# Kernel optimization log

Hardware: AMD Instinct MI355X
Metric: run time of the kernel (lower is better)

Reference implementation:

```python
import jax, jax.numpy as jnp
import numpy as np

NHEAD = 8
TOPKS = [16, 8]  # coarse -> fine (indexed by loop i over reversed pyramids)


def _gather_kv(t, idx):
    # t: [b, M, nh, d], idx: [b, N, K, nh] -> gathered [b, N, K, nh, d]
    b, M, nh, d = t.shape
    bi = jnp.arange(b)[:, None, None, None]
    hi = jnp.arange(nh)[None, None, None, :]
    return t[bi, idx, hi]


def _process_level(query, key, value, topk_pos, topk_prev, topk):
    # query: [b, c, h0, w0]; key/value: [b, c, h1, w1] with h1=h0, w1=w0
    bs, c, h0, w0 = query.shape
    _, _, h1, w1 = key.shape
    nh = NHEAD
    d = c // nh
    N = (h0 // 2) * (w0 // 2)
    # b c h w -> b (h w) nh d
    k = key.reshape(bs, c, h1 * w1).transpose(0, 2, 1).reshape(bs, h1 * w1, nh, d)
    v = value.reshape(bs, c, h1 * w1).transpose(0, 2, 1).reshape(bs, h1 * w1, nh, d)
    # b c (h 2) (w 2) -> b (h w) 4 nh d  (2x2 query groups)
    q = query.reshape(bs, c, h0 // 2, 2, w0 // 2, 2)
    q = q.transpose(0, 2, 4, 3, 5, 1).reshape(bs, N, 4, nh, d)
    # expand each coarse candidate position into its 2x2 children in the key grid
    tp = topk_pos * 2  # [2, b, N, Kp, nh]
    idx = jnp.stack([(tp[0] + x) * w1 + (tp[1] + y)
                     for x in (0, 1) for y in (0, 1)], axis=3)  # [b,N,Kp,4,nh]
    K = topk_prev * 4
    idx = idx.reshape(bs, N, K, nh)
    # sparse scores: QK[b,n,t,k,h] = <q[b,n,t,h,:], key[b, idx[b,n,k,h], h, :]>
    kg = _gather_kv(k, idx)  # [b,N,K,nh,d]
    QK = jnp.einsum('bnthd,bnkhd->bntkh', q, kg) * (d ** -0.5)
    A = jax.nn.softmax(QK, axis=-2)  # softmax over the K candidates
    # top-k over candidates (dim=-2 of A); lax.top_k works on last axis
    A_t = jnp.swapaxes(A, -1, -2)  # [b,N,4,nh,K]
    ts_t, li = jax.lax.top_k(A_t, topk)
    idx_bc = jnp.broadcast_to(jnp.swapaxes(idx, -1, -2)[:, :, None], A_t.shape)
    ti_t = jnp.take_along_axis(idx_bc, li, axis=-1)
    topk_score = jnp.swapaxes(ts_t, -1, -2)  # [b,N,4,topk,nh]
    topk_idx = jnp.swapaxes(ti_t, -1, -2)
    # value aggregation (idx is repeated over the 4 group slots in the original,
    # so a single gather is the same math): message[b,n,t,h,d]=sum_k A*v[idx]
    vg = _gather_kv(v, idx)  # [b,N,K,nh,d]
    message = jnp.einsum('bntkh,bnkhd->bnthd', A, vg)  # [b,N,4,nh,d]

    def regroup(x):  # b (h w) (t1 t2) k nh -> b (h t1 w t2) k nh
        x = x.reshape(bs, h0 // 2, w0 // 2, 2, 2, topk, nh)
        return x.transpose(0, 1, 3, 2, 4, 5, 6).reshape(bs, h0 * w0, topk, nh)

    return message, regroup(topk_score), regroup(topk_idx)


def _forward(q_fine, q_coarse, k_fine, k_coarse, v_fine, v_coarse, weight, topk_pos):
    queries = [q_fine, q_coarse]  # original list order: fine -> coarse
    keys = [k_fine, k_coarse]
    values = [v_fine, v_coarse]
    messages = []
    topk = TOPKS[0]
    tp = topk_pos
    for i, (q, k, v) in enumerate(zip(queries[::-1], keys[::-1], values[::-1])):
        w1 = k.shape[3]
        topk_prev, topk = topk, TOPKS[i]
        msg, ts, ti = _process_level(q, k, v, tp, topk_prev, topk)
        messages.append(msg)
        tp = jnp.stack([ti // w1, ti % w1])  # (row, col) in current key grid
    wsm = jax.nn.softmax(weight)

    def comb(x, H):  # b (H W) (t1 t2) h d -> b (H t1 W t2) h d, t1=t2=2
        bs, N, _, nh, d = x.shape
        W = N // H
        x = x.reshape(bs, H, W, 2, 2, nh, d).transpose(0, 1, 3, 2, 4, 5, 6)
        return x.reshape(bs, H * 2 * W * 2, nh, d)

    fm = None
    for i, m in enumerate(messages):
        if i == 0:
            fm = m * wsm[i]
        else:
            fm = fm[:, :, None] + m * wsm[i]
        # faithful to original: queries[-i] (note queries[-0] == queries[0])
        H = queries[-i].shape[2]
        fm = comb(fm, H)
    return fm  # [b, Hf*Wf, nh, d]


def setup_inputs() -> dict:
    key = jax.random.key(0)
    ks = jax.random.split(key, 8)
    f = jnp.float32
    return {
        'q_fine': jax.random.normal(ks[0], (2, 128, 128, 128), f),
        'q_coarse': jax.random.normal(ks[1], (2, 128, 64, 64), f),
        'k_fine': jax.random.normal(ks[2], (2, 128, 128, 128), f),
        'k_coarse': jax.random.normal(ks[3], (2, 128, 64, 64), f),
        'v_fine': jax.random.normal(ks[4], (2, 128, 128, 128), f),
        'v_coarse': jax.random.normal(ks[5], (2, 128, 64, 64), f),
        'weight': jax.random.normal(ks[6], (2,), f),
        'topk_pos': jax.random.randint(ks[7], (2, 2, 1024, 16, 8), 0, 32, dtype=jnp.int32),
    }


def reference(q_fine, q_coarse, k_fine, k_coarse, v_fine, v_coarse, weight, topk_pos):
    return _forward(q_fine, q_coarse, k_fine, k_coarse, v_fine, v_coarse, weight, topk_pos)
```

## Files before the change

kernel.cpp:

```cpp
#include <hip/hip_runtime.h>

#define C 128

__device__ __forceinline__ void wave_sync() {
  __builtin_amdgcn_wave_barrier();
  asm volatile("s_waitcnt lgkmcnt(0)" ::: "memory");
  __builtin_amdgcn_wave_barrier();
}

__device__ __forceinline__ void transpose_tile32(const float* __restrict__ in,
                                                 float* __restrict__ out, int P,
                                                 int tx, int chQ, int b,
                                                 float (*tile)[65]) {
  int posBase = tx * 64;
  int chBase  = chQ * 32;
  int tid = threadIdx.x;
  int lp = tid & 63;
  int lr = tid >> 6;
  const float* ip = in + (size_t)b * C * P;
  float* op = out + (size_t)b * C * P;
#pragma unroll
  for (int it = 0; it < 8; ++it) {
    int ch = lr + it * 4;
    tile[ch][lp] = ip[(size_t)(chBase + ch) * P + posBase + lp];
  }
  __syncthreads();
  int dd   = tid & 15;
  int hh2  = (tid >> 4) & 1;
  int prow = tid >> 5;
  int h = (chBase >> 4) + hh2;
#pragma unroll
  for (int it = 0; it < 8; ++it) {
    int pos = prow + it * 8;
    op[((size_t)h * P + posBase + pos) * 16 + dd] = tile[hh2 * 16 + dd][pos];
  }
}

__global__ __launch_bounds__(256) void transpose_coarse(
    const float* __restrict__ q, const float* __restrict__ k,
    const float* __restrict__ v, float* __restrict__ qo,
    float* __restrict__ ko, float* __restrict__ vo) {
  __shared__ alignas(16) float tile[32][65];
  int idx = blockIdx.x;
  int tx = idx & 63;
  int ty = (idx >> 6) % 12;
  int tz = idx / 768;
  int sel = ty >> 2;
  const float* in = sel == 0 ? q : sel == 1 ? k : v;
  float* out      = sel == 0 ? qo : sel == 1 ? ko : vo;
  transpose_tile32(in, out, 4096, tx, ty & 3, tz, tile);
}

__global__ __launch_bounds__(256) void fused_mid(
    const float* __restrict__ qf, const float* __restrict__ kf,
    const float* __restrict__ vf, float* __restrict__ qtf,
    float* __restrict__ ktf, float* __restrict__ vtf,
    const float* __restrict__ qt, const float* __restrict__ kt,
    const float* __restrict__ vt, const int* __restrict__ parents,
    float* __restrict__ mc, int* __restrict__ ti_out)
{
  __shared__ alignas(16) float lds[32 * 65];

  if (blockIdx.x >= 4096) {
    int idx = blockIdx.x - 4096;
    int tx = idx & 255;
    int ty = (idx >> 8) % 12;
    int tz = idx / 3072;
    int sel = ty >> 2;
    const float* in = sel == 0 ? qf : sel == 1 ? kf : vf;
    float* out      = sel == 0 ? qtf : sel == 1 ? ktf : vtf;
    transpose_tile32(in, out, 16384, tx, ty & 3, tz, (float (*)[65])lds);
    return;
  }

  float (*als_k)[4][17][4] = (float (*)[4][17][4])lds;
  float (*qls)[4][16]      = (float (*)[4][16])(lds + 1088);
  int   (*cofs)[64]        = (int (*)[64])    (lds + 1344);

  const int abid = blockIdx.x;
  const int lane = threadIdx.x & 63;
  const int wid  = threadIdx.x >> 6;
  const int wg = (abid & 7) * 512 + (abid >> 3);
  const int u  = wg * 4 + wid;
  const int n  = u & 1023;
  const int bh = u >> 10;
  const int b  = bh >> 3;
  const int h  = bh & 7;
  const int hb = n >> 5;
  const int wb = n & 31;
  const int hD = h * 16;

  { int t = lane >> 4, dd = lane & 15;
    int pix = (hb * 2 + (t >> 1)) * 64 + (wb * 2 + (t & 1));
    qls[wid][t][dd] = qt[((size_t)bh * 4096 + pix) * 16 + dd]; }
  int cand, off0;
  { int kp = lane >> 2, c = lane & 3;
    int r  = parents[(size_t)b * 131072          + n * 128 + kp * 8 + h];
    int cc = parents[(size_t)b * 131072 + 262144 + n * 128 + kp * 8 + h];
    cand = (2 * r + (c >> 1)) * 64 + 2 * cc + (c & 1);
    off0 = (bh * 4096 + cand) * 16;
    cofs[wid][lane] = off0; }
  wave_sync();

  const float4* kv4 = (const float4*)(kt + off0);
  float4 k0 = kv4[0], k1 = kv4[1], k2 = kv4[2], k3 = kv4[3];
  float sc[4];
#pragma unroll
  for (int t = 0; t < 4; ++t) {
    const float4* qv = (const float4*)qls[wid][t];
    float4 q0 = qv[0], q1 = qv[1], q2 = qv[2], q3 = qv[3];
    float acc = k0.x*q0.x + k0.y*q0.y + k0.z*q0.z + k0.w*q0.w
              + k1.x*q1.x + k1.y*q1.y + k1.z*q1.z + k1.w*q1.w
              + k2.x*q2.x + k2.y*q2.y + k2.z*q2.z + k2.w*q2.w
              + k3.x*q3.x + k3.y*q3.y + k3.z*q3.z + k3.w*q3.w;
    sc[t] = acc * 0.25f;
  }

  float mx[4], ex[4], sm[4], a[4];
#pragma unroll
  for (int t = 0; t < 4; ++t) mx[t] = sc[t];
#pragma unroll
  for (int off = 32; off >= 1; off >>= 1)
#pragma unroll
    for (int t = 0; t < 4; ++t) mx[t] = fmaxf(mx[t], __shfl_xor(mx[t], off));
#pragma unroll
  for (int t = 0; t < 4; ++t) { ex[t] = __expf(sc[t] - mx[t]); sm[t] = ex[t]; }
#pragma unroll
  for (int off = 32; off >= 1; off >>= 1)
#pragma unroll
    for (int t = 0; t < 4; ++t) sm[t] += __shfl_xor(sm[t], off);
#pragma unroll
  for (int t = 0; t < 4; ++t) a[t] = ex[t] / sm[t];
  *(float4*)&als_k[wid][lane >> 4][lane & 15][0] = make_float4(a[0], a[1], a[2], a[3]);

  {
    unsigned uu[4];
#pragma unroll
    for (int t = 0; t < 4; ++t) uu[t] = __float_as_uint(a[t]);
    unsigned T0 = 0, T1 = 0, T2 = 0, T3 = 0;
    for (int bit = 30; bit >= 0; --bit) {
      unsigned m = 1u << bit;
      unsigned c0 = T0 | m, c1 = T1 | m, c2 = T2 | m, c3 = T3 | m;
      if (__popcll(__ballot(uu[0] >= c0)) >= 16) T0 = c0;
      if (__popcll(__ballot(uu[1] >= c1)) >= 16) T1 = c1;
      if (__popcll(__ballot(uu[2] >= c2)) >= 16) T2 = c2;
      if (__popcll(__ballot(uu[3] >= c3)) >= 16) T3 = c3;
    }
    unsigned Tv[4] = {T0, T1, T2, T3};
    unsigned long long lower = (1ull << lane) - 1ull;
#pragma unroll
    for (int tt = 0; tt < 4; ++tt) {
      unsigned uv = uu[tt], T = Tv[tt];
      unsigned long long gt = __ballot(uv > T);
      unsigned long long eq = __ballot(uv == T);
      int ngt = __popcll(gt);
      bool sel = (uv > T) ||
                 ((uv == T) && (ngt + (int)__popcll(eq & lower) < 16));
      unsigned long long selm = __ballot(sel);
      int slot = __popcll(selm & lower);
      if (sel) {
        int n1 = (2 * hb + (tt >> 1)) * 64 + 2 * wb + (tt & 1);
        ti_out[((size_t)bh * 4096 + n1) * 16 + slot] = cand;
      }
    }
  }
  wave_sync();

  {
    const int g = lane >> 4, dd = lane & 15;
    float acc0 = 0.f, acc1 = 0.f, acc2 = 0.f, acc3 = 0.f;
#pragma unroll
    for (int k4 = 0; k4 < 16; k4 += 4) {
      int4 cv = *(const int4*)&cofs[wid][g * 16 + k4];
      float4 a0 = *(const float4*)&als_k[wid][g][k4 + 0][0];
      float4 a1 = *(const float4*)&als_k[wid][g][k4 + 1][0];
      float4 a2 = *(const float4*)&als_k[wid][g][k4 + 2][0];
      float4 a3 = *(const float4*)&als_k[wid][g][k4 + 3][0];
      float v0 = vt[cv.x + dd];
      float v1 = vt[cv.y + dd];
      float v2 = vt[cv.z + dd];
      float v3 = vt[cv.w + dd];
      acc0 += a0.x * v0; acc1 += a0.y * v0; acc2 += a0.z * v0; acc3 += a0.w * v0;
      acc0 += a1.x * v1; acc1 += a1.y * v1; acc2 += a1.z * v1; acc3 += a1.w * v1;
      acc0 += a2.x * v2; acc1 += a2.y * v2; acc2 += a2.z * v2; acc3 += a2.w * v2;
      acc0 += a3.x * v3; acc1 += a3.y * v3; acc2 += a3.z * v3; acc3 += a3.w * v3;
    }
    acc0 += __shfl_xor(acc0, 16); acc0 += __shfl_xor(acc0, 32);
    acc1 += __shfl_xor(acc1, 16); acc1 += __shfl_xor(acc1, 32);
    acc2 += __shfl_xor(acc2, 16); acc2 += __shfl_xor(acc2, 32);
    acc3 += __shfl_xor(acc3, 16); acc3 += __shfl_xor(acc3, 32);
    float msg = (g & 2) ? ((g & 1) ? acc3 : acc2) : ((g & 1) ? acc1 : acc0);
    int m = hb * 128 + (wb >> 3) * 32 + (g >> 1) * 16 + (wb & 7) * 2 + (g & 1);
    mc[(b * 4096 + m) * C + hD + dd] = msg;
  }
}

__global__ __launch_bounds__(256, 6) void attn_fine2(
    const float* __restrict__ qt, const float* __restrict__ kt,
    const float* __restrict__ vt, const int* __restrict__ tin,
    const float* __restrict__ mc, const float* __restrict__ weight,
    float* __restrict__ out)
{
  __shared__ alignas(16) float als_k[4][2][4][17][4];
  __shared__ alignas(16) float qls[4][2][4][16];
  __shared__ alignas(16) int   cofs[4][2][64];

  const int lane = threadIdx.x & 63;
  const int wid  = threadIdx.x >> 6;
  const int wg = (blockIdx.x & 7) * 1024 + (blockIdx.x >> 3);
  const int p  = wg * 4 + wid;
  const int wb2 = p & 31;
  const int hb  = (p >> 5) & 63;
  const int h   = (p >> 11) & 7;
  const int b   = p >> 14;
  const int bh  = b * 8 + h;
  const int nA  = hb * 64 + wb2 * 2;
  const int hD  = h * 16;

  { int t = lane >> 4, dd = lane & 15;
    int rowq = (hb * 2 + (t >> 1)) * 128;
    qls[wid][0][t][dd] = qt[(unsigned)(((unsigned)bh * 16384 + rowq + wb2 * 4     + (t & 1)) * 16 + dd)];
    qls[wid][1][t][dd] = qt[(unsigned)(((unsigned)bh * 16384 + rowq + wb2 * 4 + 2 + (t & 1)) * 16 + dd)];
  }
  int off0A, off0B;
  { int kp = lane >> 2, c = lane & 3;
    int tA = tin[(unsigned)(((unsigned)bh * 4096 + nA    ) * 16 + kp)];
    int tB = tin[(unsigned)(((unsigned)bh * 4096 + nA + 1) * 16 + kp)];
    int candA = (2 * (tA >> 6) + (c >> 1)) * 128 + 2 * (tA & 63) + (c & 1);
    int candB = (2 * (tB >> 6) + (c >> 1)) * 128 + 2 * (tB & 63) + (c & 1);
    off0A = (bh * 16384 + candA) * 16;
    off0B = (bh * 16384 + candB) * 16;
    cofs[wid][0][lane] = off0A;
    cofs[wid][1][lane] = off0B;
  }
  wave_sync();

  float4 kA0, kA1, kA2, kA3, kB0, kB1, kB2, kB3;
  { const float4* kv = (const float4*)&kt[(unsigned)off0A];
    kA0 = kv[0]; kA1 = kv[1]; kA2 = kv[2]; kA3 = kv[3]; }
  { const float4* kv = (const float4*)&kt[(unsigned)off0B];
    kB0 = kv[0]; kB1 = kv[1]; kB2 = kv[2]; kB3 = kv[3]; }

  float ex0[4], ex1[4];
#pragma unroll
  for (int t = 0; t < 4; ++t) {
    { const float4* qv = (const float4*)qls[wid][0][t];
      float4 q0 = qv[0], q1 = qv[1], q2 = qv[2], q3 = qv[3];
      float acc = kA0.x*q0.x + kA0.y*q0.y + kA0.z*q0.z + kA0.w*q0.w
                + kA1.x*q1.x + kA1.y*q1.y + kA1.z*q1.z + kA1.w*q1.w
                + kA2.x*q2.x + kA2.y*q2.y + kA2.z*q2.z + kA2.w*q2.w
                + kA3.x*q3.x + kA3.y*q3.y + kA3.z*q3.z + kA3.w*q3.w;
      ex0[t] = __expf(acc * 0.25f); }
    { const float4* qv = (const float4*)qls[wid][1][t];
      float4 q0 = qv[0], q1 = qv[1], q2 = qv[2], q3 = qv[3];
      float acc = kB0.x*q0.x + kB0.y*q0.y + kB0.z*q0.z + kB0.w*q0.w
                + kB1.x*q1.x + kB1.y*q1.y + kB1.z*q1.z + kB1.w*q1.w
                + kB2.x*q2.x + kB2.y*q2.y + kB2.z*q2.z + kB2.w*q2.w
                + kB3.x*q3.x + kB3.y*q3.y + kB3.z*q3.z + kB3.w*q3.w;
      ex1[t] = __expf(acc * 0.25f); }
  }
  *(float4*)&als_k[wid][0][lane >> 4][lane & 15][0] = make_float4(ex0[0], ex0[1], ex0[2], ex0[3]);
  *(float4*)&als_k[wid][1][lane >> 4][lane & 15][0] = make_float4(ex1[0], ex1[1], ex1[2], ex1[3]);
  wave_sync();

  const int g = lane >> 4, dd = lane & 15;
  float mcvA = mc[(unsigned)(((unsigned)b * 4096 + nA    ) * 128 + hD + dd)];
  float mcvB = mc[(unsigned)(((unsigned)b * 4096 + nA + 1) * 128 + hD + dd)];

  float aA0 = 0, aA1 = 0, aA2 = 0, aA3 = 0;
  float aB0 = 0, aB1 = 0, aB2 = 0, aB3 = 0;
#pragma unroll
  for (int k4 = 0; k4 < 16; k4 += 4) {
    int4 cvA = *(const int4*)&cofs[wid][0][g * 16 + k4];
    int4 cvB = *(const int4*)&cofs[wid][1][g * 16 + k4];
    float vA0 = vt[(unsigned)(cvA.x + dd)], vA1 = vt[(unsigned)(cvA.y + dd)];
    float vA2 = vt[(unsigned)(cvA.z + dd)], vA3 = vt[(unsigned)(cvA.w + dd)];
    float vB0 = vt[(unsigned)(cvB.x + dd)], vB1 = vt[(unsigned)(cvB.y + dd)];
    float vB2 = vt[(unsigned)(cvB.z + dd)], vB3 = vt[(unsigned)(cvB.w + dd)];
    float4 wA0 = *(const float4*)&als_k[wid][0][g][k4 + 0][0];
    float4 wA1 = *(const float4*)&als_k[wid][0][g][k4 + 1][0];
    float4 wA2 = *(const float4*)&als_k[wid][0][g][k4 + 2][0];
    float4 wA3 = *(const float4*)&als_k[wid][0][g][k4 + 3][0];
    float4 wB0 = *(const float4*)&als_k[wid][1][g][k4 + 0][0];
    float4 wB1 = *(const float4*)&als_k[wid][1][g][k4 + 1][0];
    float4 wB2 = *(const float4*)&als_k[wid][1][g][k4 + 2][0];
    float4 wB3 = *(const float4*)&als_k[wid][1][g][k4 + 3][0];
    aA0 += wA0.x * vA0; aA1 += wA0.y * vA0; aA2 += wA0.z * vA0; aA3 += wA0.w * vA0;
    aA0 += wA1.x * vA1; aA1 += wA1.y * vA1; aA2 += wA1.z * vA1; aA3 += wA1.w * vA1;
    aA0 += wA2.x * vA2; aA1 += wA2.y * vA2; aA2 += wA2.z * vA2; aA3 += wA2.w * vA2;
    aA0 += wA3.x * vA3; aA1 += wA3.y * vA3; aA2 += wA3.z * vA3; aA3 += wA3.w * vA3;
    aB0 += wB0.x * vB0; aB1 += wB0.y * vB0; aB2 += wB0.z * vB0; aB3 += wB0.w * vB0;
    aB0 += wB1.x * vB1; aB1 += wB1.y * vB1; aB2 += wB1.z * vB1; aB3 += wB1.w * vB1;
    aB0 += wB2.x * vB2; aB1 += wB2.y * vB2; aB2 += wB2.z * vB2; aB3 += wB2.w * vB2;
    aB0 += wB3.x * vB3; aB1 += wB3.y * vB3; aB2 += wB3.z * vB3; aB3 += wB3.w * vB3;
  }

  float smA[4], smB[4];
#pragma unroll
  for (int t = 0; t < 4; ++t) { smA[t] = ex0[t]; smB[t] = ex1[t]; }
#pragma unroll
  for (int off = 32; off >= 1; off >>= 1)
#pragma unroll
    for (int t = 0; t < 4; ++t) {
      smA[t] += __shfl_xor(smA[t], off);
      smB[t] += __shfl_xor(smB[t], off);
    }

  aA0 += __shfl_xor(aA0, 16); aA0 += __shfl_xor(aA0, 32);
  aA1 += __shfl_xor(aA1, 16); aA1 += __shfl_xor(aA1, 32);
  aA2 += __shfl_xor(aA2, 16); aA2 += __shfl_xor(aA2, 32);
  aA3 += __shfl_xor(aA3, 16); aA3 += __shfl_xor(aA3, 32);
  aB0 += __shfl_xor(aB0, 16); aB0 += __shfl_xor(aB0, 32);
  aB1 += __shfl_xor(aB1, 16); aB1 += __shfl_xor(aB1, 32);
  aB2 += __shfl_xor(aB2, 16); aB2 += __shfl_xor(aB2, 32);
  aB3 += __shfl_xor(aB3, 16); aB3 += __shfl_xor(aB3, 32);

  float msgA = (g & 2) ? ((g & 1) ? aA3 : aA2) : ((g & 1) ? aA1 : aA0);
  float msgB = (g & 2) ? ((g & 1) ? aB3 : aB2) : ((g & 1) ? aB1 : aB0);
  float smvA = (g & 2) ? ((g & 1) ? smA[3] : smA[2]) : ((g & 1) ? smA[1] : smA[0]);
  float smvB = (g & 2) ? ((g & 1) ? smB[3] : smB[2]) : ((g & 1) ? smB[1] : smB[0]);
  msgA /= smvA;
  msgB /= smvB;

  float w0 = weight[0], w1 = weight[1];
  float wm = fmaxf(w0, w1);
  float e0 = __expf(w0 - wm), e1 = __expf(w1 - wm);
  float inv = 1.0f / (e0 + e1);
  int rowq = (hb * 2 + (g >> 1)) * 128;
  out[((size_t)b * 16384 + rowq + wb2 * 4     + (g & 1)) * C + hD + dd] =
      (e0 * inv) * mcvA + (e1 * inv) * msgA;
  out[((size_t)b * 16384 + rowq + wb2 * 4 + 2 + (g & 1)) * C + hD + dd] =
      (e0 * inv) * mcvB + (e1 * inv) * msgB;
}

extern "C" void kernel_launch(void* const* d_in, const int* in_sizes, int n_in,
                              void* d_out, int out_size, void* d_ws, size_t ws_size,
                              hipStream_t stream) {
  const float* q_fine   = (const float*)d_in[0];
  const float* q_coarse = (const float*)d_in[1];
  const float* k_fine   = (const float*)d_in[2];
  const float* k_coarse = (const float*)d_in[3];
  const float* v_fine   = (const float*)d_in[4];
  const float* v_coarse = (const float*)d_in[5];
  const float* weight   = (const float*)d_in[6];
  const int*   topk_pos = (const int*)d_in[7];
  float* out = (float*)d_out;

  const int PF = 16384, PC = 4096;
  float* ws   = (float*)d_ws;
  float* qt_f = ws;
  float* kt_f = qt_f + 2 * PF * C;
  float* vt_f = kt_f + 2 * PF * C;
  float* qt_c = vt_f + 2 * PF * C;
  float* kt_c = qt_c + 2 * PC * C;
  float* vt_c = kt_c + 2 * PC * C;
  float* mc   = vt_c + 2 * PC * C;
  int*   ti   = (int*)(mc + 2 * 4096 * C);

  dim3 blk(256);
  transpose_coarse<<<1536, blk, 0, stream>>>(q_coarse, k_coarse, v_coarse,
                                             qt_c, kt_c, vt_c);
  fused_mid<<<4096 + 6144, blk, 0, stream>>>(q_fine, k_fine, v_fine,
                                             qt_f, kt_f, vt_f,
                                             qt_c, kt_c, vt_c, topk_pos, mc, ti);
  attn_fine2<<<8192, blk, 0, stream>>>(qt_f, kt_f, vt_f, ti, mc, weight, out);
}
```

Before: 93.88 us.

## Process four coarse cells per wave in fine attention kernel

The fine-level attention kernel now gives each wave a 2x2 block of four coarse query groups instead of two, and launches half as many blocks. The aim is more independent gathers in flight per wave and lower per-wave setup cost, with block-to-data mapping giving spatial locality over a 4x4 pixel tile. The cost is more registers and LDS per block and the removal of the occupancy hint in launch bounds, which may lower occupancy.

```diff
diff --git a/kernel.cpp b/kernel.cpp
--- a/kernel.cpp
+++ b/kernel.cpp
@@ -195,142 +195,188 @@
   }
 }
 
-__global__ __launch_bounds__(256, 6) void attn_fine2(
+__global__ __launch_bounds__(256) void attn_fine4(
     const float* __restrict__ qt, const float* __restrict__ kt,
     const float* __restrict__ vt, const int* __restrict__ tin,
     const float* __restrict__ mc, const float* __restrict__ weight,
     float* __restrict__ out)
 {
-  __shared__ alignas(16) float als_k[4][2][4][17][4];
-  __shared__ alignas(16) float qls[4][2][4][16];
-  __shared__ alignas(16) int   cofs[4][2][64];
+  __shared__ alignas(16) float als_k[4][4][4][17][4];
+  __shared__ alignas(16) float qls[4][4][4][16];
+  __shared__ alignas(16) int   cofs[4][4][64];
 
   const int lane = threadIdx.x & 63;
   const int wid  = threadIdx.x >> 6;
-  const int wg = (blockIdx.x & 7) * 1024 + (blockIdx.x >> 3);
-  const int p  = wg * 4 + wid;
-  const int wb2 = p & 31;
-  const int hb  = (p >> 5) & 63;
-  const int h   = (p >> 11) & 7;
-  const int b   = p >> 14;
-  const int bh  = b * 8 + h;
-  const int nA  = hb * 64 + wb2 * 2;
-  const int hD  = h * 16;
+  const int wg = (blockIdx.x & 7) * 512 + (blockIdx.x >> 3);
+  const int qd = wg * 4 + wid;
+  const int wc = qd & 31;
+  const int hc = (qd >> 5) & 31;
+  const int h  = (qd >> 10) & 7;
+  const int b  = qd >> 13;
+  const int bh = b * 8 + h;
+  const int hD = h * 16;
 
   { int t = lane >> 4, dd = lane & 15;
-    int rowq = (hb * 2 + (t >> 1)) * 128;
-    qls[wid][0][t][dd] = qt[(unsigned)(((unsigned)bh * 16384 + rowq + wb2 * 4     + (t & 1)) * 16 + dd)];
-    qls[wid][1][t][dd] = qt[(unsigned)(((unsigned)bh * 16384 + rowq + wb2 * 4 + 2 + (t & 1)) * 16 + dd)];
-  }
-  int off0A, off0B;
+    int prow0 = 4 * hc + (t >> 1);
+    int pcol0 = 4 * wc + (t & 1);
+#pragma unroll
+    for (int i = 0; i < 2; ++i)
+#pragma unroll
+      for (int j = 0; j < 2; ++j)
+        qls[wid][i * 2 + j][t][dd] =
+          qt[(unsigned)(((unsigned)bh * 16384 + (prow0 + 2 * i) * 128 + pcol0 + 2 * j) * 16 + dd)];
+  }
   { int kp = lane >> 2, c = lane & 3;
-    int tA = tin[(unsigned)(((unsigned)bh * 4096 + nA    ) * 16 + kp)];
-    int tB = tin[(unsigned)(((unsigned)bh * 4096 + nA + 1) * 16 + kp)];
-    int candA = (2 * (tA >> 6) + (c >> 1)) * 128 + 2 * (tA & 63) + (c & 1);
-    int candB = (2 * (tB >> 6) + (c >> 1)) * 128 + 2 * (tB & 63) + (c & 1);
-    off0A = (bh * 16384 + candA) * 16;
-    off0B = (bh * 16384 + candB) * 16;
-    cofs[wid][0][lane] = off0A;
-    cofs[wid][1][lane] = off0B;
+#pragma unroll
+    for (int u = 0; u < 4; ++u) {
+      int n1 = (2 * hc + (u >> 1)) * 64 + 2 * wc + (u & 1);
+      int tv = tin[(unsigned)(((unsigned)bh * 4096 + n1) * 16 + kp)];
+      int cand = (2 * (tv >> 6) + (c >> 1)) * 128 + 2 * (tv & 63) + (c & 1);
+      cofs[wid][u][lane] = (bh * 16384 + cand) * 16;
+    }
   }
   wave_sync();
 
-  float4 kA0, kA1, kA2, kA3, kB0, kB1, kB2, kB3;
-  { const float4* kv = (const float4*)&kt[(unsigned)off0A];
-    kA0 = kv[0]; kA1 = kv[1]; kA2 = kv[2]; kA3 = kv[3]; }
-  { const float4* kv = (const float4*)&kt[(unsigned)off0B];
-    kB0 = kv[0]; kB1 = kv[1]; kB2 = kv[2]; kB3 = kv[3]; }
-
-  float ex0[4], ex1[4];
-#pragma unroll
-  for (int t = 0; t < 4; ++t) {
-    { const float4* qv = (const float4*)qls[wid][0][t];
-      float4 q0 = qv[0], q1 = qv[1], q2 = qv[2], q3 = qv[3];
-      float acc = kA0.x*q0.x + kA0.y*q0.y + kA0.z*q0.z + kA0.w*q0.w
-                + kA1.x*q1.x + kA1.y*q1.y + kA1.z*q1.z + kA1.w*q1.w
-                + kA2.x*q2.x + kA2.y*q2.y + kA2.z*q2.z + kA2.w*q2.w
-                + kA3.x*q3.x + kA3.y*q3.y + kA3.z*q3.z + kA3.w*q3.w;
-      ex0[t] = __expf(acc * 0.25f); }
-    { const float4* qv = (const float4*)qls[wid][1][t];
-      float4 q0 = qv[0], q1 = qv[1], q2 = qv[2], q3 = qv[3];
-      float acc = kB0.x*q0.x + kB0.y*q0.y + kB0.z*q0.z + kB0.w*q0.w
-                + kB1.x*q1.x + kB1.y*q1.y + kB1.z*q1.z + kB1.w*q1.w
-                + kB2.x*q2.x + kB2.y*q2.y + kB2.z*q2.z + kB2.w*q2.w
-                + kB3.x*q3.x + kB3.y*q3.y + kB3.z*q3.z + kB3.w*q3.w;
-      ex1[t] = __expf(acc * 0.25f); }
+  float ex0[4], ex1[4], ex2[4], ex3[4];
+  {
+    int offA = cofs[wid][0][lane], offB = cofs[wid][1][lane];
+    float4 kA0, kA1, kA2, kA3, kB0, kB1, kB2, kB3;
+    { const float4* kv = (const float4*)&kt[(unsigned)offA];
+      kA0 = kv[0]; kA1 = kv[1]; kA2 = kv[2]; kA3 = kv[3]; }
+    { const float4* kv = (const float4*)&kt[(unsigned)offB];
+      kB0 = kv[0]; kB1 = kv[1]; kB2 = kv[2]; kB3 = kv[3]; }
+#pragma unroll
+    for (int t = 0; t < 4; ++t) {
+      { const float4* qv = (const float4*)qls[wid][0][t];
+        float4 q0 = qv[0], q1 = qv[1], q2 = qv[2], q3 = qv[3];
+        float acc = kA0.x*q0.x + kA0.y*q0.y + kA0.z*q0.z + kA0.w*q0.w
+                  + kA1.x*q1.x + kA1.y*q1.y + kA1.z*q1.z + kA1.w*q1.w
+                  + kA2.x*q2.x + kA2.y*q2.y + kA2.z*q2.z + kA2.w*q2.w
+                  + kA3.x*q3.x + kA3.y*q3.y + kA3.z*q3.z + kA3.w*q3.w;
+        ex0[t] = __expf(acc * 0.25f); }
+      { const float4* qv = (const float4*)qls[wid][1][t];
+        float4 q0 = qv[0], q1 = qv[1], q2 = qv[2], q3 = qv[3];
+        float acc = kB0.x*q0.x + kB0.y*q0.y + kB0.z*q0.z + kB0.w*q0.w
+                  + kB1.x*q1.x + kB1.y*q1.y + kB1.z*q1.z + kB1.w*q1.w
+                  + kB2.x*q2.x + kB2.y*q2.y + kB2.z*q2.z + kB2.w*q2.w
+                  + kB3.x*q3.x + kB3.y*q3.y + kB3.z*q3.z + kB3.w*q3.w;
+        ex1[t] = __expf(acc * 0.25f); }
+    }
   }
   *(float4*)&als_k[wid][0][lane >> 4][lane & 15][0] = make_float4(ex0[0], ex0[1], ex0[2], ex0[3]);
   *(float4*)&als_k[wid][1][lane >> 4][lane & 15][0] = make_float4(ex1[0], ex1[1], ex1[2], ex1[3]);
+  {
+    int offA = cofs[wid][2][lane], offB = cofs[wid][3][lane];
+    float4 kA0, kA1, kA2, kA3, kB0, kB1, kB2, kB3;
+    { const float4* kv = (const float4*)&kt[(unsigned)offA];
+      kA0 = kv[0]; kA1 = kv[1]; kA2 = kv[2]; kA3 = kv[3]; }
+    { const float4* kv = (const float4*)&kt[(unsigned)offB];
+      kB0 = kv[0]; kB1 = kv[1]; kB2 = kv[2]; kB3 = kv[3]; }
+#pragma unroll
+    for (int t = 0; t < 4; ++t) {
+      { const float4* qv = (const float4*)qls[wid][2][t];
+        float4 q0 = qv[0], q1 = qv[1], q2 = qv[2], q3 = qv[3];
+        float acc = kA0.x*q0.x + kA0.y*q0.y + kA0.z*q0.z + kA0.w*q0.w
+                  + kA1.x*q1.x + kA1.y*q1.y + kA1.z*q1.z + kA1.w*q1.w
+                  + kA2.x*q2.x + kA2.y*q2.y + kA2.z*q2.z + kA2.w*q2.w
+                  + kA3.x*q3.x + kA3.y*q3.y + kA3.z*q3.z + kA3.w*q3.w;
+        ex2[t] = __expf(acc * 0.25f); }
+      { const float4* qv = (const float4*)qls[wid][3][t];
+        float4 q0 = qv[0], q1 = qv[1], q2 = qv[2], q3 = qv[3];
+        float acc = kB0.x*q0.x + kB0.y*q0.y + kB0.z*q0.z + kB0.w*q0.w
+                  + kB1.x*q1.x + kB1.y*q1.y + kB1.z*q1.z + kB1.w*q1.w
+                  + kB2.x*q2.x + kB2.y*q2.y + kB2.z*q2.z + kB2.w*q2.w
+                  + kB3.x*q3.x + kB3.y*q3.y + kB3.z*q3.z + kB3.w*q3.w;
+        ex3[t] = __expf(acc * 0.25f); }
+    }
+  }
+  *(float4*)&als_k[wid][2][lane >> 4][lane & 15][0] = make_float4(ex2[0], ex2[1], ex2[2], ex2[3]);
+  *(float4*)&als_k[wid][3][lane >> 4][lane & 15][0] = make_float4(ex3[0], ex3[1], ex3[2], ex3[3]);
   wave_sync();
 
   const int g = lane >> 4, dd = lane & 15;
-  float mcvA = mc[(unsigned)(((unsigned)b * 4096 + nA    ) * 128 + hD + dd)];
-  float mcvB = mc[(unsigned)(((unsigned)b * 4096 + nA + 1) * 128 + hD + dd)];
-
-  float aA0 = 0, aA1 = 0, aA2 = 0, aA3 = 0;
-  float aB0 = 0, aB1 = 0, aB2 = 0, aB3 = 0;
-#pragma unroll
-  for (int k4 = 0; k4 < 16; k4 += 4) {
-    int4 cvA = *(const int4*)&cofs[wid][0][g * 16 + k4];
-    int4 cvB = *(const int4*)&cofs[wid][1][g * 16 + k4];
-    float vA0 = vt[(unsigned)(cvA.x + dd)], vA1 = vt[(unsigned)(cvA.y + dd)];
-    float vA2 = vt[(unsigned)(cvA.z + dd)], vA3 = vt[(unsigned)(cvA.w + dd)];
-    float vB0 = vt[(unsigned)(cvB.x + dd)], vB1 = vt[(unsigned)(cvB.y + dd)];
-    float vB2 = vt[(unsigned)(cvB.z + dd)], vB3 = vt[(unsigned)(cvB.w + dd)];
-    float4 wA0 = *(const float4*)&als_k[wid][0][g][k4 + 0][0];
-    float4 wA1 = *(const float4*)&als_k[wid][0][g][k4 + 1][0];
-    float4 wA2 = *(const float4*)&als_k[wid][0][g][k4 + 2][0];
-    float4 wA3 = *(const float4*)&als_k[wid][0][g][k4 + 3][0];
-    float4 wB0 = *(const float4*)&als_k[wid][1][g][k4 + 0][0];
-    float4 wB1 = *(const float4*)&als_k[wid][1][g][k4 + 1][0];
-    float4 wB2 = *(const float4*)&als_k[wid][1][g][k4 + 2][0];
-    float4 wB3 = *(const float4*)&als_k[wid][1][g][k4 + 3][0];
-    aA0 += wA0.x * vA0; aA1 += wA0.y * vA0; aA2 += wA0.z * vA0; aA3 += wA0.w * vA0;
-    aA0 += wA1.x * vA1; aA1 += wA1.y * vA1; aA2 += wA1.z * vA1; aA3 += wA1.w * vA1;
-    aA0 += wA2.x * vA2; aA1 += wA2.y * vA2; aA2 += wA2.z * vA2; aA3 += wA2.w * vA2;
-    aA0 += wA3.x * vA3; aA1 += wA3.y * vA3; aA2 += wA3.z * vA3; aA3 += wA3.w * vA3;
-    aB0 += wB0.x * vB0; aB1 += wB0.y * vB0; aB2 += wB0.z * vB0; aB3 += wB0.w * vB0;
-    aB0 += wB1.x * vB1; aB1 += wB1.y * vB1; aB2 += wB1.z * vB1; aB3 += wB1.w * vB1;
-    aB0 += wB2.x * vB2; aB1 += wB2.y * vB2; aB2 += wB2.z * vB2; aB3 += wB2.w * vB2;
-    aB0 += wB3.x * vB3; aB1 += wB3.y * vB3; aB2 += wB3.z * vB3; aB3 += wB3.w * vB3;
-  }
-
-  float smA[4], smB[4];
-#pragma unroll
-  for (int t = 0; t < 4; ++t) { smA[t] = ex0[t]; smB[t] = ex1[t]; }
-#pragma unroll
-  for (int off = 32; off >= 1; off >>= 1)
-#pragma unroll
-    for (int t = 0; t < 4; ++t) {
-      smA[t] += __shfl_xor(smA[t], off);
-      smB[t] += __shfl_xor(smB[t], off);
-    }
-
-  aA0 += __shfl_xor(aA0, 16); aA0 += __shfl_xor(aA0, 32);
-  aA1 += __shfl_xor(aA1, 16); aA1 += __shfl_xor(aA1, 32);
-  aA2 += __shfl_xor(aA2, 16); aA2 += __shfl_xor(aA2, 32);
-  aA3 += __shfl_xor(aA3, 16); aA3 += __shfl_xor(aA3, 32);
-  aB0 += __shfl_xor(aB0, 16); aB0 += __shfl_xor(aB0, 32);
-  aB1 += __shfl_xor(aB1, 16); aB1 += __shfl_xor(aB1, 32);
-  aB2 += __shfl_xor(aB2, 16); aB2 += __shfl_xor(aB2, 32);
-  aB3 += __shfl_xor(aB3, 16); aB3 += __shfl_xor(aB3, 32);
-
-  float msgA = (g & 2) ? ((g & 1) ? aA3 : aA2) : ((g & 1) ? aA1 : aA0);
-  float msgB = (g & 2) ? ((g & 1) ? aB3 : aB2) : ((g & 1) ? aB1 : aB0);
-  float smvA = (g & 2) ? ((g & 1) ? smA[3] : smA[2]) : ((g & 1) ? smA[1] : smA[0]);
-  float smvB = (g & 2) ? ((g & 1) ? smB[3] : smB[2]) : ((g & 1) ? smB[1] : smB[0]);
-  msgA /= smvA;
-  msgB /= smvB;
+
+  float mcv[4];
+#pragma unroll
+  for (int u = 0; u < 4; ++u) {
+    int n1 = (2 * hc + (u >> 1)) * 64 + 2 * wc + (u & 1);
+    mcv[u] = mc[(unsigned)(((unsigned)b * 4096 + n1) * 128 + hD + dd)];
+  }
+
+  float smv[4];
+  {
+    float s0[4], s1[4], s2[4], s3[4];
+#pragma unroll
+    for (int t = 0; t < 4; ++t) { s0[t] = ex0[t]; s1[t] = ex1[t]; s2[t] = ex2[t]; s3[t] = ex3[t]; }
+#pragma unroll
+    for (int off = 32; off >= 1; off >>= 1)
+#pragma unroll
+      for (int t = 0; t < 4; ++t) {
+        s0[t] += __shfl_xor(s0[t], off);
+        s1[t] += __shfl_xor(s1[t], off);
+        s2[t] += __shfl_xor(s2[t], off);
+        s3[t] += __shfl_xor(s3[t], off);
+      }
+    smv[0] = (g & 2) ? ((g & 1) ? s0[3] : s0[2]) : ((g & 1) ? s0[1] : s0[0]);
+    smv[1] = (g & 2) ? ((g & 1) ? s1[3] : s1[2]) : ((g & 1) ? s1[1] : s1[0]);
+    smv[2] = (g & 2) ? ((g & 1) ? s2[3] : s2[2]) : ((g & 1) ? s2[1] : s2[0]);
+    smv[3] = (g & 2) ? ((g & 1) ? s3[3] : s3[2]) : ((g & 1) ? s3[1] : s3[0]);
+  }
+
+  float msg[4];
+#pragma unroll
+  for (int pp = 0; pp < 2; ++pp) {
+    const int uA = pp * 2, uB = pp * 2 + 1;
+    float aA0 = 0, aA1 = 0, aA2 = 0, aA3 = 0;
+    float aB0 = 0, aB1 = 0, aB2 = 0, aB3 = 0;
+#pragma unroll
+    for (int k4 = 0; k4 < 16; k4 += 4) {
+      int4 cvA = *(const int4*)&cofs[wid][uA][g * 16 + k4];
+      int4 cvB = *(const int4*)&cofs[wid][uB][g * 16 + k4];
+      float vA0 = vt[(unsigned)(cvA.x + dd)], vA1 = vt[(unsigned)(cvA.y + dd)];
+      float vA2 = vt[(unsigned)(cvA.z + dd)], vA3 = vt[(unsigned)(cvA.w + dd)];
+      float vB0 = vt[(unsigned)(cvB.x + dd)], vB1 = vt[(unsigned)(cvB.y + dd)];
+      float vB2 = vt[(unsigned)(cvB.z + dd)], vB3 = vt[(unsigned)(cvB.w + dd)];
+      float4 wA0 = *(const float4*)&als_k[wid][uA][g][k4 + 0][0];
+      float4 wA1 = *(const float4*)&als_k[wid][uA][g][k4 + 1][0];
+      float4 wA2 = *(const float4*)&als_k[wid][uA][g][k4 + 2][0];
+      float4 wA3 = *(const float4*)&als_k[wid][uA][g][k4 + 3][0];
+      float4 wB0 = *(const float4*)&als_k[wid][uB][g][k4 + 0][0];
+      float4 wB1 = *(const float4*)&als_k[wid][uB][g][k4 + 1][0];
+      float4 wB2 = *(const float4*)&als_k[wid][uB][g][k4 + 2][0];
+      float4 wB3 = *(const float4*)&als_k[wid][uB][g][k4 + 3][0];
+      aA0 += wA0.x * vA0; aA1 += wA0.y * vA0; aA2 += wA0.z * vA0; aA3 += wA0.w * vA0;
+      aA0 += wA1.x * vA1; aA1 += wA1.y * vA1; aA2 += wA1.z * vA1; aA3 += wA1.w * vA1;
+      aA0 += wA2.x * vA2; aA1 += wA2.y * vA2; aA2 += wA2.z * vA2; aA3 += wA2.w * vA2;
+      aA0 += wA3.x * vA3; aA1 += wA3.y * vA3; aA2 += wA3.z * vA3; aA3 += wA3.w * vA3;
+      aB0 += wB0.x * vB0; aB1 += wB0.y * vB0; aB2 += wB0.z * vB0; aB3 += wB0.w * vB0;
+      aB0 += wB1.x * vB1; aB1 += wB1.y * vB1; aB2 += wB1.z * vB1; aB3 += wB1.w * vB1;
+      aB0 += wB2.x * vB2; aB1 += wB2.y * vB2; aB2 += wB2.z * vB2; aB3 += wB2.w * vB2;
+      aB0 += wB3.x * vB3; aB1 += wB3.y * vB3; aB2 += wB3.z * vB3; aB3 += wB3.w * vB3;
+    }
+    aA0 += __shfl_xor(aA0, 16); aA0 += __shfl_xor(aA0, 32);
+    aA1 += __shfl_xor(aA1, 16); aA1 += __shfl_xor(aA1, 32);
+    aA2 += __shfl_xor(aA2, 16); aA2 += __shfl_xor(aA2, 32);
+    aA3 += __shfl_xor(aA3, 16); aA3 += __shfl_xor(aA3, 32);
+    aB0 += __shfl_xor(aB0, 16); aB0 += __shfl_xor(aB0, 32);
+    aB1 += __shfl_xor(aB1, 16); aB1 += __shfl_xor(aB1, 32);
+    aB2 += __shfl_xor(aB2, 16); aB2 += __shfl_xor(aB2, 32);
+    aB3 += __shfl_xor(aB3, 16); aB3 += __shfl_xor(aB3, 32);
+    msg[uA] = ((g & 2) ? ((g & 1) ? aA3 : aA2) : ((g & 1) ? aA1 : aA0)) / smv[uA];
+    msg[uB] = ((g & 2) ? ((g & 1) ? aB3 : aB2) : ((g & 1) ? aB1 : aB0)) / smv[uB];
+  }
 
   float w0 = weight[0], w1 = weight[1];
   float wm = fmaxf(w0, w1);
   float e0 = __expf(w0 - wm), e1 = __expf(w1 - wm);
   float inv = 1.0f / (e0 + e1);
-  int rowq = (hb * 2 + (g >> 1)) * 128;
-  out[((size_t)b * 16384 + rowq + wb2 * 4     + (g & 1)) * C + hD + dd] =
-      (e0 * inv) * mcvA + (e1 * inv) * msgA;
-  out[((size_t)b * 16384 + rowq + wb2 * 4 + 2 + (g & 1)) * C + hD + dd] =
-      (e0 * inv) * mcvB + (e1 * inv) * msgB;
+#pragma unroll
+  for (int u = 0; u < 4; ++u) {
+    int prow = 4 * hc + 2 * (u >> 1) + (g >> 1);
+    int pcol = 4 * wc + 2 * (u & 1) + (g & 1);
+    out[((size_t)b * 16384 + prow * 128 + pcol) * C + hD + dd] =
+        (e0 * inv) * mcv[u] + (e1 * inv) * msg[u];
+  }
 }
 
 extern "C" void kernel_launch(void* const* d_in, const int* in_sizes, int n_in,
@@ -363,5 +409,5 @@
   fused_mid<<<4096 + 6144, blk, 0, stream>>>(q_fine, k_fine, v_fine,
                                              qt_f, kt_f, vt_f,
                                              qt_c, kt_c, vt_c, topk_pos, mc, ti);
-  attn_fine2<<<8192, blk, 0, stream>>>(qt_f, kt_f, vt_f, ti, mc, weight, out);
-}
+  attn_fine4<<<4096, blk, 0, stream>>>(qt_f, kt_f, vt_f, ti, mc, weight, out);
+}
```

Result: slower. 96.62 us (+2.9%).
